# Kernel optimization log

Measured on AMD Instinct MI355X. Metric: run time of the kernel, lower is better.

The kernel has to match this reference:

```python
import jax, jax.numpy as jnp
import numpy as np

NV2, NV1, NV0 = 163842, 40962, 10242  # icosphere res 7/6/5 vertex counts
DEG = 6
ALPHA = 0.3  # LeakyReLU slope (torch default in EdgeUNet)


def edgeconv(feat, src, tgt, W, b, nv):
    """EdgeConv: gather neighbor diffs -> 1x1 conv (linear) -> scatter-mean -> LeakyReLU."""
    local = feat[tgt]                       # [E, C]
    nb = feat[src]                          # [E, C]
    x = jnp.concatenate([local, nb - local], axis=-1)   # [E, 2C]
    y = x @ W.T + b                         # [E, Cout] (Conv1d k=1 == linear)
    s = jax.ops.segment_sum(y, tgt, num_segments=nv)
    cnt = jax.ops.segment_sum(jnp.ones((tgt.shape[0], 1), y.dtype), tgt, num_segments=nv)
    red = s / jnp.maximum(cnt, 1.0)         # mean with include_self=False; degree-0 rows stay 0
    return jnp.where(red >= 0, red, ALPHA * red)


def setup_inputs() -> dict:
    key = jax.random.key(0)
    ks = jax.random.split(key, 16)

    def edges(k, nv):
        E = nv * DEG
        src = jax.random.randint(k, (E,), 0, nv)
        tgt = jnp.repeat(jnp.arange(nv), DEG)   # sorted targets, degree DEG each
        return src, tgt

    src2, tgt2 = edges(ks[0], NV2)
    src1, tgt1 = edges(ks[1], NV1)
    src0, tgt0 = edges(ks[2], NV0)
    # child->parent pooling maps; identity prefix guarantees full coverage
    p21 = jnp.concatenate([jnp.arange(NV1), jax.random.randint(ks[3], (NV2 - NV1,), 0, NV1)])
    p10 = jnp.concatenate([jnp.arange(NV0), jax.random.randint(ks[4], (NV1 - NV0,), 0, NV0)])
    features = jax.random.normal(ks[5], (NV2, 16), jnp.float32)

    def wb(k, cin, cout):
        kw, kb = jax.random.split(k)
        s = 1.0 / np.sqrt(cin)
        W = jax.random.uniform(kw, (cout, cin), jnp.float32, -s, s)
        b = jax.random.uniform(kb, (cout,), jnp.float32, -s, s)
        return W, b

    w_enc0, b_enc0 = wb(ks[6], 2 * 16, 32)
    w_enc1, b_enc1 = wb(ks[7], 2 * 32, 64)
    w_enc2, b_enc2 = wb(ks[8], 2 * 64, 128)
    w_dec0, b_dec0 = wb(ks[9], 2 * (128 + 64), 64)
    w_dec1, b_dec1 = wb(ks[10], 2 * (64 + 32), 32)

    return dict(features=features, src2=src2, tgt2=tgt2, src1=src1, tgt1=tgt1,
                src0=src0, tgt0=tgt0, p21=p21, p10=p10,
                w_enc0=w_enc0, b_enc0=b_enc0, w_enc1=w_enc1, b_enc1=b_enc1,
                w_enc2=w_enc2, b_enc2=b_enc2, w_dec0=w_dec0, b_dec0=b_dec0,
                w_dec1=w_dec1, b_dec1=b_dec1)


def reference(features, src2, tgt2, src1, tgt1, src0, tgt0, p21, p10,
              w_enc0, b_enc0, w_enc1, b_enc1, w_enc2, b_enc2,
              w_dec0, b_dec0, w_dec1, b_dec1):
    # encoder
    f2 = edgeconv(features, src2, tgt2, w_enc0, b_enc0, NV2)   # [NV2, 32]
    f1 = jax.ops.segment_max(f2, p21, num_segments=NV1)        # max pooling
    f1 = edgeconv(f1, src1, tgt1, w_enc1, b_enc1, NV1)         # [NV1, 64]
    f0 = jax.ops.segment_max(f1, p10, num_segments=NV0)
    f0 = edgeconv(f0, src0, tgt0, w_enc2, b_enc2, NV0)         # [NV0, 128]
    # decoder: upsample (parent gather) + skip concat + EdgeConv
    u1 = jnp.concatenate([f0[p10], f1], axis=-1)               # [NV1, 192]
    d1 = edgeconv(u1, src1, tgt1, w_dec0, b_dec0, NV1)         # [NV1, 64]
    u2 = jnp.concatenate([d1[p21], f2], axis=-1)               # [NV2, 96]
    out = edgeconv(u2, src2, tgt2, w_dec1, b_dec1, NV2)        # [NV2, 32]
    return out
```

## Files before the change

kernel.cpp:

```cpp
#include <hip/hip_runtime.h>

#define NV2 163842
#define NV1 40962
#define NV0 10242

using u32 = unsigned int;
using u16 = unsigned short;

typedef __attribute__((ext_vector_type(8))) short bf16x8;
typedef __attribute__((ext_vector_type(4))) float f32x4;

__device__ __forceinline__ u16 f2bf(float f) {
  u32 u = __float_as_uint(f);
  return (u16)((u + 0x7FFFu + ((u >> 16) & 1u)) >> 16);
}
__device__ __forceinline__ void unpack8(uint4 u, float* f) {
  f[0] = __uint_as_float(u.x << 16); f[1] = __uint_as_float(u.x & 0xFFFF0000u);
  f[2] = __uint_as_float(u.y << 16); f[3] = __uint_as_float(u.y & 0xFFFF0000u);
  f[4] = __uint_as_float(u.z << 16); f[5] = __uint_as_float(u.z & 0xFFFF0000u);
  f[6] = __uint_as_float(u.w << 16); f[7] = __uint_as_float(u.w & 0xFFFF0000u);
}
__device__ __forceinline__ uint4 pack8(const float* f) {
  uint4 o;
  o.x = (u32)f2bf(f[0]) | ((u32)f2bf(f[1]) << 16);
  o.y = (u32)f2bf(f[2]) | ((u32)f2bf(f[3]) << 16);
  o.z = (u32)f2bf(f[4]) | ((u32)f2bf(f[5]) << 16);
  o.w = (u32)f2bf(f[6]) | ((u32)f2bf(f[7]) << 16);
  return o;
}
__device__ __forceinline__ u16 enc16(u16 h) {
  return (h & 0x8000u) ? (u16)~h : (u16)(h | 0x8000u);
}
__device__ __forceinline__ u16 dec16(u16 e) {
  return (e & 0x8000u) ? (u16)(e & 0x7FFFu) : (u16)~e;
}

__device__ __forceinline__ float enc_w(const float* __restrict__ W, int C, int i) {
  int j = i / (2 * C), k = i % (2 * C);
  float v = W[(size_t)j * 2 * C + k];
  if (k < C) v -= W[(size_t)j * 2 * C + C + k];
  return v;
}
__device__ __forceinline__ float dec_w(const float* __restrict__ W, int C, int COUT, int i) {
  int j = i / C, k = i % C;
  if (j < COUT) return W[(size_t)j * 2 * C + C + k];
  return W[(size_t)(j - COUT) * 2 * C + k] - W[(size_t)(j - COUT) * 2 * C + C + k];
}

__global__ __launch_bounds__(256) void prep_all_k(
    const float* __restrict__ features, u16* __restrict__ featb,
    u32* __restrict__ pb1, u32* __restrict__ pb0,
    const float* __restrict__ w_enc0, u16* __restrict__ We0,
    const float* __restrict__ w_enc1, u16* __restrict__ We1,
    const float* __restrict__ w_enc2, u16* __restrict__ We2,
    const float* __restrict__ w_dec0, u16* __restrict__ Wd0,
    const float* __restrict__ w_dec1, u16* __restrict__ Wd1) {
  long i = (long)blockIdx.x * 256 + threadIdx.x;
  const long n_cvt = (long)NV2 * 16;
  if (i < n_cvt) { featb[i] = f2bf(features[i]); return; }
  i -= n_cvt;
  const long n_pb1 = (long)NV1 * 32;
  if (i < n_pb1) { pb1[i] = 0u; return; }
  i -= n_pb1;
  const long n_pb0 = (long)NV0 * 64;
  if (i < n_pb0) { pb0[i] = 0u; return; }
  i -= n_pb0;
  if (i < 32 * 32)   { We0[i] = f2bf(enc_w(w_enc0, 16, (int)i)); return; }
  i -= 32 * 32;
  if (i < 64 * 64)   { We1[i] = f2bf(enc_w(w_enc1, 32, (int)i)); return; }
  i -= 64 * 64;
  if (i < 128 * 128) { We2[i] = f2bf(enc_w(w_enc2, 64, (int)i)); return; }
  i -= 128 * 128;
  if (i < 128 * 192) { Wd0[i] = f2bf(dec_w(w_dec0, 192, 64, (int)i)); return; }
  i -= 128 * 192;
  if (i < 64 * 96)   { Wd1[i] = f2bf(dec_w(w_dec1, 96, 32, (int)i)); return; }
}

__global__ __launch_bounds__(256) void pool_decode_k(const u32* __restrict__ buf,
                                                     const u16* __restrict__ own,
                                                     u16* __restrict__ outbf, int n) {
  int i = blockIdx.x * 256 + threadIdx.x;
  if (i < n) {
    u16 e = (u16)(buf[i] >> 16);
    u16 eo = enc16(own[i]);
    outbf[i] = dec16(e > eo ? e : eo);
  }
}

template <int C, int COUT, bool POOL>
__global__ __launch_bounds__(256) void gemm_enc_k(
    const u16* __restrict__ fb, const int* __restrict__ src,
    const u16* __restrict__ Wt, const float* __restrict__ bias,
    u16* __restrict__ outb, u32* __restrict__ pb,
    const int* __restrict__ pmap, int nparent, int nv) {
  constexpr int K = 2 * C;
  constexpr int NT = COUT / 16;
  const int w = threadIdx.x >> 6, lane = threadIdx.x & 63;
  const int lr = lane & 15, lg = lane >> 4;
  const int vbase = blockIdx.x * 64 + w * 16;
  int arow = vbase + lr; if (arow >= nv) arow = nv - 1;

  int sidx[6];
#pragma unroll
  for (int kk = 0; kk < 6; ++kk) sidx[kk] = src[(size_t)arow * 6 + kk];

  f32x4 acc[NT] = {};
#pragma unroll
  for (int kt = 0; kt < K; kt += 32) {
    const int k = kt + lg * 8;
    bf16x8 a;
    if (k < C) {
      a = *(const bf16x8*)&fb[(size_t)arow * C + k];
    } else {
      const int c0 = k - C;
      float s[8] = {0.f, 0.f, 0.f, 0.f, 0.f, 0.f, 0.f, 0.f};
#pragma unroll
      for (int kk = 0; kk < 6; ++kk) {
        float nb[8];
        unpack8(*(const uint4*)&fb[(size_t)sidx[kk] * C + c0], nb);
#pragma unroll
        for (int j = 0; j < 8; ++j) s[j] += nb[j];
      }
#pragma unroll
      for (int j = 0; j < 8; ++j) s[j] *= (1.f / 6.f);
      uint4 p = pack8(s);
      a = *(bf16x8*)&p;
    }
#pragma unroll
    for (int nt = 0; nt < NT; ++nt) {
      bf16x8 b = *(const bf16x8*)&Wt[(size_t)(nt * 16 + lr) * K + k];
      acc[nt] = __builtin_amdgcn_mfma_f32_16x16x32_bf16(a, b, acc[nt], 0, 0, 0);
    }
  }

  int prow[4];
  if constexpr (POOL) {
#pragma unroll
    for (int r = 0; r < 4; ++r) {
      int v = vbase + lg * 4 + r;
      prow[r] = (v < nv && v >= nparent) ? pmap[v] : -1;
    }
  }
#pragma unroll
  for (int nt = 0; nt < NT; ++nt) {
#pragma unroll
    for (int r = 0; r < 4; ++r) {
      int v = vbase + lg * 4 + r;
      if (v < nv) {
        int n = nt * 16 + lr;
        float y = acc[nt][r] + bias[n];
        y = (y >= 0.f) ? y : 0.3f * y;
        u16 hb = f2bf(y);
        outb[(size_t)v * COUT + n] = hb;
        if constexpr (POOL)
          if (prow[r] >= 0)
            atomicMax(&pb[(size_t)prow[r] * COUT + n], ((u32)enc16(hb)) << 16);
      }
    }
  }
}

template <int CA, int CB, int COUT>
__global__ __launch_bounds__(256) void gemm_dec_k(
    const u16* __restrict__ Ab, const int* __restrict__ map,
    const u16* __restrict__ Bb, const u16* __restrict__ Wt,
    u16* __restrict__ h, u16* __restrict__ zb, int nv) {
  constexpr int K = CA + CB;
  constexpr int N = 2 * COUT;
  constexpr int NT = N / 16;
  const int w = threadIdx.x >> 6, lane = threadIdx.x & 63;
  const int lr = lane & 15, lg = lane >> 4;
  const int vbase = blockIdx.x * 64 + w * 16;
  int arow = vbase + lr; if (arow >= nv) arow = nv - 1;
  const int m = map[arow];

  f32x4 acc[NT] = {};
#pragma unroll
  for (int kt = 0; kt < K; kt += 32) {
    int k = kt + lg * 8;
    bf16x8 a = (k < CA) ? *(const bf16x8*)&Ab[(size_t)m * CA + k]
                        : *(const bf16x8*)&Bb[(size_t)arow * CB + (k - CA)];
#pragma unroll
    for (int nt = 0; nt < NT; ++nt) {
      bf16x8 b = *(const bf16x8*)&Wt[(size_t)(nt * 16 + lr) * K + k];
      acc[nt] = __builtin_amdgcn_mfma_f32_16x16x32_bf16(a, b, acc[nt], 0, 0, 0);
    }
  }
#pragma unroll
  for (int nt = 0; nt < NT; ++nt) {
#pragma unroll
    for (int r = 0; r < 4; ++r) {
      int v = vbase + lg * 4 + r;
      if (v < nv) {
        int n = nt * 16 + lr;
        u16 val = f2bf(acc[nt][r]);
        if (n < COUT) h[(size_t)v * COUT + n] = val;
        else          zb[(size_t)v * COUT + (n - COUT)] = val;
      }
    }
  }
}

template <int COUT, bool OUT32, bool OUTB>
__global__ __launch_bounds__(256) void combine_k(
    const u16* __restrict__ h, const u16* __restrict__ zb,
    const int* __restrict__ src, const float* __restrict__ bias,
    float* __restrict__ out32, u16* __restrict__ outb, int nv) {
  constexpr int TPV = COUT / 8;
  int gid = blockIdx.x * 256 + threadIdx.x;
  if (gid >= nv * TPV) return;
  int v = gid / TPV, c0 = (gid % TPV) * 8;
  const int* __restrict__ sp = src + (size_t)v * 6;
  float s[8] = {0.f, 0.f, 0.f, 0.f, 0.f, 0.f, 0.f, 0.f};
#pragma unroll
  for (int k = 0; k < 6; ++k) {
    float nb[8];
    unpack8(*(const uint4*)&h[(size_t)sp[k] * COUT + c0], nb);
#pragma unroll
    for (int j = 0; j < 8; ++j) s[j] += nb[j];
  }
  constexpr float inv6 = 1.f / 6.f;
  float zl[8];
  unpack8(*(const uint4*)&zb[(size_t)v * COUT + c0], zl);
  float4 b0 = *(const float4*)&bias[c0];
  float4 b1 = *(const float4*)&bias[c0 + 4];
  float y[8];
  y[0] = zl[0] + s[0] * inv6 + b0.x; y[1] = zl[1] + s[1] * inv6 + b0.y;
  y[2] = zl[2] + s[2] * inv6 + b0.z; y[3] = zl[3] + s[3] * inv6 + b0.w;
  y[4] = zl[4] + s[4] * inv6 + b1.x; y[5] = zl[5] + s[5] * inv6 + b1.y;
  y[6] = zl[6] + s[6] * inv6 + b1.z; y[7] = zl[7] + s[7] * inv6 + b1.w;
#pragma unroll
  for (int j = 0; j < 8; ++j) y[j] = (y[j] >= 0.f) ? y[j] : 0.3f * y[j];
  if constexpr (OUT32) {
    *(float4*)&out32[(size_t)v * COUT + c0]     = make_float4(y[0], y[1], y[2], y[3]);
    *(float4*)&out32[(size_t)v * COUT + c0 + 4] = make_float4(y[4], y[5], y[6], y[7]);
  }
  if constexpr (OUTB) *(uint4*)&outb[(size_t)v * COUT + c0] = pack8(y);
}

extern "C" void kernel_launch(void* const* d_in, const int* in_sizes, int n_in,
                              void* d_out, int out_size, void* d_ws, size_t ws_size,
                              hipStream_t stream) {
  const float* features = (const float*)d_in[0];
  const int* src2 = (const int*)d_in[1];
  const int* src1 = (const int*)d_in[3];
  const int* src0 = (const int*)d_in[5];
  const int* p21 = (const int*)d_in[7];
  const int* p10 = (const int*)d_in[8];
  const float* w_enc0 = (const float*)d_in[9];
  const float* b_enc0 = (const float*)d_in[10];
  const float* w_enc1 = (const float*)d_in[11];
  const float* b_enc1 = (const float*)d_in[12];
  const float* w_enc2 = (const float*)d_in[13];
  const float* b_enc2 = (const float*)d_in[14];
  const float* w_dec0 = (const float*)d_in[15];
  const float* b_dec0 = (const float*)d_in[16];
  const float* w_dec1 = (const float*)d_in[17];
  const float* b_dec1 = (const float*)d_in[18];

  u16* featb = (u16*)d_ws;
  u16* f2b   = featb + (size_t)NV2 * 16;
  u16* f1pb  = f2b   + (size_t)NV2 * 32;
  u16* f1b   = f1pb  + (size_t)NV1 * 32;
  u16* f0pb  = f1b   + (size_t)NV1 * 64;
  u16* f0b   = f0pb  + (size_t)NV0 * 64;
  u16* h1b   = f0b   + (size_t)NV0 * 128;
  u16* d1b   = h1b   + (size_t)NV1 * 64;
  u16* h2b   = d1b   + (size_t)NV1 * 64;
  u16* z1b   = h2b   + (size_t)NV2 * 32;
  u16* z2b   = z1b   + (size_t)NV1 * 64;
  u16* We0   = z2b   + (size_t)NV2 * 32;
  u16* We1   = We0 + 32 * 32;
  u16* We2   = We1 + 64 * 64;
  u16* Wd0   = We2 + 128 * 128;
  u16* Wd1   = Wd0 + 128 * 192;
  u32* pb1   = (u32*)(Wd1 + 64 * 96);
  u32* pb0   = pb1 + (size_t)NV1 * 32;
  float* out = (float*)d_out;

  auto cdiv = [](long long a, long long b) { return (int)((a + b - 1) / b); };

  const long prep_n = (long)NV2 * 16 + (long)NV1 * 32 + (long)NV0 * 64 +
                      32 * 32 + 64 * 64 + 128 * 128 + 128 * 192 + 64 * 96;
  prep_all_k<<<cdiv(prep_n, 256), 256, 0, stream>>>(
      features, featb, pb1, pb0, w_enc0, We0, w_enc1, We1, w_enc2, We2,
      w_dec0, Wd0, w_dec1, Wd1);

  gemm_enc_k<16, 32, true><<<cdiv(NV2, 64), 256, 0, stream>>>(
      featb, src2, We0, b_enc0, f2b, pb1, p21, NV1, NV2);
  pool_decode_k<<<cdiv((size_t)NV1 * 32, 256), 256, 0, stream>>>(
      pb1, f2b, f1pb, NV1 * 32);
  gemm_enc_k<32, 64, true><<<cdiv(NV1, 64), 256, 0, stream>>>(
      f1pb, src1, We1, b_enc1, f1b, pb0, p10, NV0, NV1);
  pool_decode_k<<<cdiv((size_t)NV0 * 64, 256), 256, 0, stream>>>(
      pb0, f1b, f0pb, NV0 * 64);
  gemm_enc_k<64, 128, false><<<cdiv(NV0, 64), 256, 0, stream>>>(
      f0pb, src0, We2, b_enc2, f0b, nullptr, nullptr, 0, NV0);
  gemm_dec_k<128, 64, 64><<<cdiv(NV1, 64), 256, 0, stream>>>(
      f0b, p10, f1b, Wd0, h1b, z1b, NV1);
  combine_k<64, false, true><<<cdiv((size_t)NV1 * 8, 256), 256, 0, stream>>>(
      h1b, z1b, src1, b_dec0, nullptr, d1b, NV1);
  gemm_dec_k<64, 32, 32><<<cdiv(NV2, 64), 256, 0, stream>>>(
      d1b, p21, f2b, Wd1, h2b, z2b, NV2);
  combine_k<32, true, false><<<cdiv((size_t)NV2 * 4, 256), 256, 0, stream>>>(
      h2b, z2b, src2, b_dec1, out, nullptr, NV2);
}
```

Baseline: 131.6 us.

## Replace atomicMax pooling with child-list build and gather-based max pooling

Removes the per-channel atomicMax into encoded parent buffers and the decode kernel. Extra blocks in the encoder GEMM launch record each parent's children into a bounded list using one atomicAdd per child. A gather kernel then computes the max over the parent's own row and its listed children. This cuts atomic traffic and buffer zeroing. The cost is irregular gathers, and children beyond CAP=24 per parent would be dropped.

```diff
diff --git a/kernel.cpp b/kernel.cpp
--- a/kernel.cpp
+++ b/kernel.cpp
@@ -3,6 +3,7 @@
 #define NV2 163842
 #define NV1 40962
 #define NV0 10242
+#define CAP 24
 
 using u32 = unsigned int;
 using u16 = unsigned short;
@@ -28,12 +29,6 @@
   o.w = (u32)f2bf(f[6]) | ((u32)f2bf(f[7]) << 16);
   return o;
 }
-__device__ __forceinline__ u16 enc16(u16 h) {
-  return (h & 0x8000u) ? (u16)~h : (u16)(h | 0x8000u);
-}
-__device__ __forceinline__ u16 dec16(u16 e) {
-  return (e & 0x8000u) ? (u16)(e & 0x7FFFu) : (u16)~e;
-}
 
 __device__ __forceinline__ float enc_w(const float* __restrict__ W, int C, int i) {
   int j = i / (2 * C), k = i % (2 * C);
@@ -49,7 +44,7 @@
 
 __global__ __launch_bounds__(256) void prep_all_k(
     const float* __restrict__ features, u16* __restrict__ featb,
-    u32* __restrict__ pb1, u32* __restrict__ pb0,
+    u32* __restrict__ cnt1, u32* __restrict__ cnt0,
     const float* __restrict__ w_enc0, u16* __restrict__ We0,
     const float* __restrict__ w_enc1, u16* __restrict__ We1,
     const float* __restrict__ w_enc2, u16* __restrict__ We2,
@@ -59,12 +54,10 @@
   const long n_cvt = (long)NV2 * 16;
   if (i < n_cvt) { featb[i] = f2bf(features[i]); return; }
   i -= n_cvt;
-  const long n_pb1 = (long)NV1 * 32;
-  if (i < n_pb1) { pb1[i] = 0u; return; }
-  i -= n_pb1;
-  const long n_pb0 = (long)NV0 * 64;
-  if (i < n_pb0) { pb0[i] = 0u; return; }
-  i -= n_pb0;
+  if (i < NV1) { cnt1[i] = 0u; return; }
+  i -= NV1;
+  if (i < NV0) { cnt0[i] = 0u; return; }
+  i -= NV0;
   if (i < 32 * 32)   { We0[i] = f2bf(enc_w(w_enc0, 16, (int)i)); return; }
   i -= 32 * 32;
   if (i < 64 * 64)   { We1[i] = f2bf(enc_w(w_enc1, 32, (int)i)); return; }
@@ -76,23 +69,48 @@
   if (i < 64 * 96)   { Wd1[i] = f2bf(dec_w(w_dec1, 96, 32, (int)i)); return; }
 }
 
-__global__ __launch_bounds__(256) void pool_decode_k(const u32* __restrict__ buf,
-                                                     const u16* __restrict__ own,
-                                                     u16* __restrict__ outbf, int n) {
-  int i = blockIdx.x * 256 + threadIdx.x;
-  if (i < n) {
-    u16 e = (u16)(buf[i] >> 16);
-    u16 eo = enc16(own[i]);
-    outbf[i] = dec16(e > eo ? e : eo);
-  }
-}
-
-template <int C, int COUT, bool POOL>
+template <int C>
+__global__ __launch_bounds__(256) void poolg_k(const u16* __restrict__ child,
+                                               const u32* __restrict__ cnt,
+                                               const int* __restrict__ kid,
+                                               u16* __restrict__ outp, int nparent) {
+  constexpr int TPV = C / 8;
+  int gid = blockIdx.x * 256 + threadIdx.x;
+  if (gid >= nparent * TPV) return;
+  int p = gid / TPV, c0 = (gid % TPV) * 8;
+  float m[8];
+  unpack8(*(const uint4*)&child[(size_t)p * C + c0], m);
+  int n = (int)min(cnt[p], (u32)CAP);
+  for (int j = 0; j < n; ++j) {
+    int v = kid[(size_t)p * CAP + j];
+    float nb[8];
+    unpack8(*(const uint4*)&child[(size_t)v * C + c0], nb);
+#pragma unroll
+    for (int q = 0; q < 8; ++q) m[q] = fmaxf(m[q], nb[q]);
+  }
+  *(uint4*)&outp[(size_t)p * C + c0] = pack8(m);
+}
+
+template <int C, int COUT, bool BUILD>
 __global__ __launch_bounds__(256) void gemm_enc_k(
     const u16* __restrict__ fb, const int* __restrict__ src,
     const u16* __restrict__ Wt, const float* __restrict__ bias,
-    u16* __restrict__ outb, u32* __restrict__ pb,
-    const int* __restrict__ pmap, int nparent, int nv) {
+    u16* __restrict__ outb, const int* __restrict__ pmap,
+    u32* __restrict__ cnt, int* __restrict__ kid,
+    int nparent, int nv, int gemm_blocks) {
+  if constexpr (BUILD) {
+    if ((int)blockIdx.x >= gemm_blocks) {
+      int idx = ((int)blockIdx.x - gemm_blocks) * 256 + threadIdx.x;
+      int tail = nv - nparent;
+      if (idx < tail) {
+        int v = nparent + idx;
+        int p = pmap[v];
+        u32 slot = atomicAdd(&cnt[p], 1u);
+        if (slot < (u32)CAP) kid[(size_t)p * CAP + slot] = v;
+      }
+      return;
+    }
+  }
   constexpr int K = 2 * C;
   constexpr int NT = COUT / 16;
   const int w = threadIdx.x >> 6, lane = threadIdx.x & 63;
@@ -132,15 +150,6 @@
       acc[nt] = __builtin_amdgcn_mfma_f32_16x16x32_bf16(a, b, acc[nt], 0, 0, 0);
     }
   }
-
-  int prow[4];
-  if constexpr (POOL) {
-#pragma unroll
-    for (int r = 0; r < 4; ++r) {
-      int v = vbase + lg * 4 + r;
-      prow[r] = (v < nv && v >= nparent) ? pmap[v] : -1;
-    }
-  }
 #pragma unroll
   for (int nt = 0; nt < NT; ++nt) {
 #pragma unroll
@@ -150,11 +159,7 @@
         int n = nt * 16 + lr;
         float y = acc[nt][r] + bias[n];
         y = (y >= 0.f) ? y : 0.3f * y;
-        u16 hb = f2bf(y);
-        outb[(size_t)v * COUT + n] = hb;
-        if constexpr (POOL)
-          if (prow[r] >= 0)
-            atomicMax(&pb[(size_t)prow[r] * COUT + n], ((u32)enc16(hb)) << 16);
+        outb[(size_t)v * COUT + n] = f2bf(y);
       }
     }
   }
@@ -274,28 +279,36 @@
   u16* We2   = We1 + 64 * 64;
   u16* Wd0   = We2 + 128 * 128;
   u16* Wd1   = Wd0 + 128 * 192;
-  u32* pb1   = (u32*)(Wd1 + 64 * 96);
-  u32* pb0   = pb1 + (size_t)NV1 * 32;
+  u32* cnt1  = (u32*)(Wd1 + 64 * 96);
+  u32* cnt0  = cnt1 + NV1;
+  int* kid1  = (int*)(cnt0 + NV0);
+  int* kid0  = kid1 + (size_t)NV1 * CAP;
   float* out = (float*)d_out;
 
   auto cdiv = [](long long a, long long b) { return (int)((a + b - 1) / b); };
 
-  const long prep_n = (long)NV2 * 16 + (long)NV1 * 32 + (long)NV0 * 64 +
+  const long prep_n = (long)NV2 * 16 + NV1 + NV0 +
                       32 * 32 + 64 * 64 + 128 * 128 + 128 * 192 + 64 * 96;
   prep_all_k<<<cdiv(prep_n, 256), 256, 0, stream>>>(
-      features, featb, pb1, pb0, w_enc0, We0, w_enc1, We1, w_enc2, We2,
+      features, featb, cnt1, cnt0, w_enc0, We0, w_enc1, We1, w_enc2, We2,
       w_dec0, Wd0, w_dec1, Wd1);
 
-  gemm_enc_k<16, 32, true><<<cdiv(NV2, 64), 256, 0, stream>>>(
-      featb, src2, We0, b_enc0, f2b, pb1, p21, NV1, NV2);
-  pool_decode_k<<<cdiv((size_t)NV1 * 32, 256), 256, 0, stream>>>(
-      pb1, f2b, f1pb, NV1 * 32);
-  gemm_enc_k<32, 64, true><<<cdiv(NV1, 64), 256, 0, stream>>>(
-      f1pb, src1, We1, b_enc1, f1b, pb0, p10, NV0, NV1);
-  pool_decode_k<<<cdiv((size_t)NV0 * 64, 256), 256, 0, stream>>>(
-      pb0, f1b, f0pb, NV0 * 64);
+  {
+    int gb = cdiv(NV2, 64), bb = cdiv(NV2 - NV1, 256);
+    gemm_enc_k<16, 32, true><<<gb + bb, 256, 0, stream>>>(
+        featb, src2, We0, b_enc0, f2b, p21, cnt1, kid1, NV1, NV2, gb);
+  }
+  poolg_k<32><<<cdiv((size_t)NV1 * 4, 256), 256, 0, stream>>>(
+      f2b, cnt1, kid1, f1pb, NV1);
+  {
+    int gb = cdiv(NV1, 64), bb = cdiv(NV1 - NV0, 256);
+    gemm_enc_k<32, 64, true><<<gb + bb, 256, 0, stream>>>(
+        f1pb, src1, We1, b_enc1, f1b, p10, cnt0, kid0, NV0, NV1, gb);
+  }
+  poolg_k<64><<<cdiv((size_t)NV0 * 8, 256), 256, 0, stream>>>(
+      f1b, cnt0, kid0, f0pb, NV0);
   gemm_enc_k<64, 128, false><<<cdiv(NV0, 64), 256, 0, stream>>>(
-      f0pb, src0, We2, b_enc2, f0b, nullptr, nullptr, 0, NV0);
+      f0pb, src0, We2, b_enc2, f0b, nullptr, nullptr, nullptr, 0, NV0, 0);
   gemm_dec_k<128, 64, 64><<<cdiv(NV1, 64), 256, 0, stream>>>(
       f0b, p10, f1b, Wd0, h1b, z1b, NV1);
   combine_k<64, false, true><<<cdiv((size_t)NV1 * 8, 256), 256, 0, stream>>>(
```

Measured after the change: 135.8 us. +3.2%, slower.
